# Optimization experiments

Hardware: AMD Instinct MI355X
Metric: run time of the kernel (lower is better)

## Reference

```python
import jax, jax.numpy as jnp
import numpy as np
from jax.scipy.special import logsumexp

EPSILON = 0.01      # Sinkhorn entropic regularization
MAX_ITERATIONS = 50 # Sinkhorn iterations (init kwarg)
NEG_INF = -1e9      # finite stand-in for log(0) to keep grads clean


def setup_inputs() -> dict:
    key = jax.random.key(0)
    k1, k2, k3 = jax.random.split(key, 3)
    B, S, P, D = 8, 2048, 1024, 2
    predictions = jax.random.normal(k1, (B, S, D), dtype=jnp.float32)
    positions = jax.random.normal(k2, (B, P, D), dtype=jnp.float32)
    labels = jax.random.randint(k3, (B, S), 0, P)
    return {"predictions": predictions, "labels": labels, "positions": positions}


def _sinkhorn_loss(predictions, positions, labels):
    B, S, D = predictions.shape
    P = positions.shape[1]
    dt = predictions.dtype

    # target weights = normalized label histogram over the P positions
    w = jnp.zeros((B, P), dt).at[jnp.arange(B)[:, None], labels].add(1.0) / S
    log_a = jnp.full((B, S), -jnp.log(jnp.asarray(S, dt)), dtype=dt)  # uniform source
    log_b = jnp.where(w > 0, jnp.log(jnp.maximum(w, 1e-30)), NEG_INF)

    # squared-Euclidean cost matrix [B, S, P]
    x2 = jnp.sum(predictions * predictions, axis=-1)  # [B,S]
    y2 = jnp.sum(positions * positions, axis=-1)      # [B,P]
    xy = jnp.einsum('bsd,bpd->bsp', predictions, positions)
    C = jnp.maximum(x2[:, :, None] + y2[:, None, :] - 2.0 * xy, 0.0)
    mK = -C / EPSILON  # log-kernel

    def step(carry, _):
        f, g = carry
        f = EPSILON * (log_a - logsumexp(mK + g[:, None, :] / EPSILON, axis=2))
        g = EPSILON * (log_b - logsumexp(mK + f[:, :, None] / EPSILON, axis=1))
        return (f, g), None

    f0 = jnp.zeros((B, S), dt)
    g0 = jnp.zeros((B, P), dt)
    (f, g), _ = jax.lax.scan(step, (f0, g0), None, length=MAX_ITERATIONS)

    # transport plan in log domain; distance = <P, C>
    logT = mK + f[:, :, None] / EPSILON + g[:, None, :] / EPSILON
    dist = jnp.sum(jnp.exp(logT) * C, axis=(1, 2))  # [B]
    return jnp.mean(dist)  # reduction='mean'


def reference(predictions, labels, positions):
    return _sinkhorn_loss(predictions, positions, labels)
```

## Files before the change

### kernel.cpp

```cpp
#include <hip/hip_runtime.h>
#include <math.h>


#define BB 8
#define SS 2048
#define PP 1024
#define NEG_INF -1e9f
#define LOG2S 11.0f
#define ITERS 50
#define K2E 144.269504088896f
#define TWOK 288.539008177792f
#define NBLK 256
#define NTHR 1024

__device__ __forceinline__ float fexp2(float x) {
  return __builtin_amdgcn_exp2f(x);
}
__device__ __forceinline__ float flog2(float x) {
  return __builtin_amdgcn_logf(x);
}

__device__ __forceinline__ float coh_load(const float* p) {
  return __hip_atomic_load((float*)p, __ATOMIC_RELAXED, __HIP_MEMORY_SCOPE_AGENT);
}
__device__ __forceinline__ void coh_store(float* p, float v) {
  __hip_atomic_store(p, v, __ATOMIC_RELAXED, __HIP_MEMORY_SCOPE_AGENT);
}
__device__ __forceinline__ int coh_loadi(const int* p) {
  return __hip_atomic_load((int*)p, __ATOMIC_RELAXED, __HIP_MEMORY_SCOPE_AGENT);
}
__device__ __forceinline__ void coh_storei(int* p, int v) {
  __hip_atomic_store(p, v, __ATOMIC_RELAXED, __HIP_MEMORY_SCOPE_AGENT);
}

__device__ __forceinline__ void batch_barrier(int* slots, int sub, int phase,
                                              int w, int lane) {
  __syncthreads();
  asm volatile("" ::: "memory");
  if (threadIdx.x == 0) coh_storei(&slots[sub], phase);
  if (w == 0) {
    for (;;) {
      int v = (lane < 32) ? coh_loadi(&slots[lane]) : 0x7fffffff;
      if (__all(v >= phase)) break;
      __builtin_amdgcn_s_sleep(1);
    }
  }
  asm volatile("" ::: "memory");
  __syncthreads();
}


__global__ __launch_bounds__(1024) void setup_kernel(
    const int* __restrict__ labels, float* __restrict__ G2,
    float* __restrict__ logb2, int* __restrict__ slots,
    float* __restrict__ out) {
  __shared__ int c[PP];
  int b = blockIdx.x;
  int t = threadIdx.x;
  c[t] = 0;
  __syncthreads();
  atomicAdd(&c[labels[b * SS + t] & (PP - 1)], 1);
  atomicAdd(&c[labels[b * SS + PP + t] & (PP - 1)], 1);
  __syncthreads();
  int cc = c[t];
  logb2[b * PP + t] = (cc > 0) ? (flog2((float)cc) - LOG2S) : NEG_INF;
  G2[b * PP + t] = 0.0f;
  if (t < 32) slots[(b << 5) + t] = 0;
  if (t == 0 && b == 0) out[0] = 0.0f;
}

__global__ __launch_bounds__(1024) void sinkhorn_persist(
    const float* __restrict__ preds, const float* __restrict__ pos,
    const float* __restrict__ logb2, float* __restrict__ F2g,
    float* __restrict__ G2g, int* __restrict__ slots,
    float* __restrict__ out) {
  __shared__ float4 shf[1032];
  __shared__ float4 shg[2064];
  __shared__ float spart;
  const int t = threadIdx.x;
  const int blk = blockIdx.x;
  const int bb = blk >> 5;
  const int sub = blk & 31;
  int* myslots = slots + (bb << 5);
  const float2* pos2 = (const float2*)pos;
  const float2* preds2 = (const float2*)preds;
  float* G2b = G2g + (bb << 10);
  float* F2b = F2g + (bb << 11);

  float yr2, xr2[2];
  {
    float2 y = pos2[(bb << 10) + t];
    yr2 = y.x * y.x + y.y * y.y;
    shf[t + (t >> 7)] = make_float4(y.x, y.y, 0.0f, 0.0f);
  }
#pragma unroll
  for (int k = 0; k < 2; ++k) {
    int e = t + (k << 10);
    float2 x = preds2[(bb << 11) + e];
    xr2[k] = x.x * x.x + x.y * x.y;
    shg[e + (e >> 7)] = make_float4(x.x, x.y, 0.0f, 0.0f);
  }

  const int w = t >> 6, lane = t & 63;
  const int frowb = (blk << 6) + (w << 2);
  float fk0[4], fk1[4], fc0[4];
#pragma unroll
  for (int r = 0; r < 4; ++r) {
    float2 fx = preds2[frowb + r];
    fk0[r] = TWOK * fx.x;
    fk1[r] = TWOK * fx.y;
    fc0[r] = fmaf(K2E, fx.x * fx.x + fx.y * fx.y, -LOG2S);
  }
  const int gcolb = (blk << 5) + (w << 1);
  float gk0[2], gk1[2], gc0[2];
#pragma unroll
  for (int c = 0; c < 2; ++c) {
    float2 gy = pos2[gcolb + c];
    gk0[c] = TWOK * gy.x;
    gk1[c] = TWOK * gy.y;
    gc0[c] = fmaf(K2E, gy.x * gy.x + gy.y * gy.y, logb2[gcolb + c]);
  }

  for (int it = 0; it < ITERS; ++it) {
    shf[t + (t >> 7)].z = fmaf(-K2E, yr2, coh_load(&G2b[t]));
    __syncthreads();
    {
      float m[4], s[4];
#pragma unroll
      for (int r = 0; r < 4; ++r) { m[r] = -3.4e38f; s[r] = 0.0f; }
#pragma unroll
      for (int ch = 0; ch < 2; ++ch) {
        float4 a[8];
#pragma unroll
        for (int i = 0; i < 8; ++i) {
          int e = (((ch << 3) + i) << 6) + lane;
          a[i] = shf[e + (e >> 7)];
        }
#pragma unroll
        for (int r = 0; r < 4; ++r) {
          float u0 = fmaf(fk0[r], a[0].x, fmaf(fk1[r], a[0].y, a[0].z));
          float u1 = fmaf(fk0[r], a[1].x, fmaf(fk1[r], a[1].y, a[1].z));
          float u2 = fmaf(fk0[r], a[2].x, fmaf(fk1[r], a[2].y, a[2].z));
          float u3 = fmaf(fk0[r], a[3].x, fmaf(fk1[r], a[3].y, a[3].z));
          float u4 = fmaf(fk0[r], a[4].x, fmaf(fk1[r], a[4].y, a[4].z));
          float u5 = fmaf(fk0[r], a[5].x, fmaf(fk1[r], a[5].y, a[5].z));
          float u6 = fmaf(fk0[r], a[6].x, fmaf(fk1[r], a[6].y, a[6].z));
          float u7 = fmaf(fk0[r], a[7].x, fmaf(fk1[r], a[7].y, a[7].z));
          float cm = fmaxf(fmaxf(fmaxf(u0, u1), fmaxf(u2, u3)),
                           fmaxf(fmaxf(u4, u5), fmaxf(u6, u7)));
          float mn = fmaxf(m[r], cm);
          float sc = fexp2(m[r] - mn);
          float sum = ((fexp2(u0 - mn) + fexp2(u1 - mn)) +
                       (fexp2(u2 - mn) + fexp2(u3 - mn))) +
                      ((fexp2(u4 - mn) + fexp2(u5 - mn)) +
                       (fexp2(u6 - mn) + fexp2(u7 - mn)));
          s[r] = fmaf(s[r], sc, sum);
          m[r] = mn;
        }
      }
      float fout = 0.0f;
#pragma unroll
      for (int r = 0; r < 4; ++r) {
        float M = m[r];
#pragma unroll
        for (int off = 1; off <= 32; off <<= 1)
          M = fmaxf(M, __shfl_xor(M, off, 64));
        float sr = s[r] * fexp2(m[r] - M);
#pragma unroll
        for (int off = 1; off <= 32; off <<= 1) sr += __shfl_xor(sr, off, 64);
        float v = fc0[r] - M - flog2(sr);
        if (lane == r) fout = v;
      }
      if (lane < 4) coh_store(&F2g[frowb + lane], fout);
    }
    batch_barrier(myslots, sub, 2 * it + 1, w, lane);

#pragma unroll
    for (int k = 0; k < 2; ++k) {
      int e = t + (k << 10);
      shg[e + (e >> 7)].z = fmaf(-K2E, xr2[k], coh_load(&F2b[e]));
    }
    __syncthreads();
    {
      float m[2], s[2];
#pragma unroll
      for (int c = 0; c < 2; ++c) { m[c] = -3.4e38f; s[c] = 0.0f; }
#pragma unroll
      for (int ch = 0; ch < 4; ++ch) {
        float4 a[8];
#pragma unroll
        for (int i = 0; i < 8; ++i) {
          int e = (((ch << 3) + i) << 6) + lane;
          a[i] = shg[e + (e >> 7)];
        }
#pragma unroll
        for (int c = 0; c < 2; ++c) {
          float u0 = fmaf(gk0[c], a[0].x, fmaf(gk1[c], a[0].y, a[0].z));
          float u1 = fmaf(gk0[c], a[1].x, fmaf(gk1[c], a[1].y, a[1].z));
          float u2 = fmaf(gk0[c], a[2].x, fmaf(gk1[c], a[2].y, a[2].z));
          float u3 = fmaf(gk0[c], a[3].x, fmaf(gk1[c], a[3].y, a[3].z));
          float u4 = fmaf(gk0[c], a[4].x, fmaf(gk1[c], a[4].y, a[4].z));
          float u5 = fmaf(gk0[c], a[5].x, fmaf(gk1[c], a[5].y, a[5].z));
          float u6 = fmaf(gk0[c], a[6].x, fmaf(gk1[c], a[6].y, a[6].z));
          float u7 = fmaf(gk0[c], a[7].x, fmaf(gk1[c], a[7].y, a[7].z));
          float cm = fmaxf(fmaxf(fmaxf(u0, u1), fmaxf(u2, u3)),
                           fmaxf(fmaxf(u4, u5), fmaxf(u6, u7)));
          float mn = fmaxf(m[c], cm);
          float sc = fexp2(m[c] - mn);
          float sum = ((fexp2(u0 - mn) + fexp2(u1 - mn)) +
                       (fexp2(u2 - mn) + fexp2(u3 - mn))) +
                      ((fexp2(u4 - mn) + fexp2(u5 - mn)) +
                       (fexp2(u6 - mn) + fexp2(u7 - mn)));
          s[c] = fmaf(s[c], sc, sum);
          m[c] = mn;
        }
      }
      float gout = 0.0f;
#pragma unroll
      for (int c = 0; c < 2; ++c) {
        float M = m[c];
#pragma unroll
        for (int off = 1; off <= 32; off <<= 1)
          M = fmaxf(M, __shfl_xor(M, off, 64));
        float sr = s[c] * fexp2(m[c] - M);
#pragma unroll
        for (int off = 1; off <= 32; off <<= 1) sr += __shfl_xor(sr, off, 64);
        float v = gc0[c] - M - flog2(sr);
        if (lane == c) gout = v;
      }
      if (lane < 2) coh_store(&G2g[gcolb + lane], gout);
    }
    batch_barrier(myslots, sub, 2 * it + 2, w, lane);
  }

  if (t == 0) spart = 0.0f;
  shf[t + (t >> 7)].z = fmaf(-K2E, yr2, coh_load(&G2b[t]));
  __syncthreads();
  float acc = 0.0f;
#pragma unroll
  for (int rr = 0; rr < 4; ++rr) {
    int row = frowb + rr;
    float2 x = preds2[row];
    float x2 = x.x * x.x + x.y * x.y;
    float qx = fmaf(-K2E, x2, coh_load(&F2g[row]));
#pragma unroll
    for (int i = 0; i < 16; ++i) {
      int p = (i << 6) + lane;
      float4 a = shf[p + (p >> 7)];
      float y2 = fmaf(a.x, a.x, a.y * a.y);
      float tt = fmaf(x.y, a.y, x.x * a.x);
      float c = fmaxf(x2 + y2 - 2.0f * tt, 0.0f);
      float v2 = fmaf(TWOK, tt, a.z + qx);
      acc = fmaf(fexp2(v2), c, acc);
    }
  }
#pragma unroll
  for (int off = 32; off; off >>= 1) acc += __shfl_xor(acc, off, 64);
  if (lane == 0) atomicAdd(&spart, acc);
  __syncthreads();
  if (t == 0) atomicAdd(out, spart * (1.0f / (float)BB));
}

extern "C" void kernel_launch(void* const* d_in, const int* in_sizes, int n_in,
                              void* d_out, int out_size, void* d_ws,
                              size_t ws_size, hipStream_t stream) {
  const float* preds = (const float*)d_in[0];
  const int* labels = (const int*)d_in[1];
  const float* pos = (const float*)d_in[2];
  float* out = (float*)d_out;
  char* ws = (char*)d_ws;
  float* G2 = (float*)(ws);
  float* F2 = (float*)(ws + 32768);
  float* logb2 = (float*)(ws + 98304);
  int* slots = (int*)(ws + 131072);

  hipLaunchKernelGGL(setup_kernel, dim3(BB), dim3(1024), 0, stream, labels, G2,
                     logb2, slots, out);
  hipLaunchKernelGGL(sinkhorn_persist, dim3(NBLK), dim3(NTHR), 0, stream,
                     preds, pos, logb2, F2, G2, slots, out);
}
```

Baseline: 611.0 us.

## Double persistent grid to 512 blocks and split row reductions across waves

Raises the persistent Sinkhorn grid from 256 to 512 blocks, so each batch now spans 64 blocks with a 64-slot barrier. Each f-row is now split across two waves and each g-column across four waves, with partial log-sum-exp results merged through a small shared-memory buffer. Per-row and per-column constants are recomputed each iteration to lower register pressure. The goal is more resident waves per CU for better latency hiding. In exchange it adds an extra __syncthreads and merge step per half-iteration, makes the barrier wider, and needs two 1024-thread blocks co-resident per CU, or the spin barrier may deadlock.

```diff
diff --git a/kernel.cpp b/kernel.cpp
--- a/kernel.cpp
+++ b/kernel.cpp
@@ -10,7 +10,7 @@
 #define ITERS 50
 #define K2E 144.269504088896f
 #define TWOK 288.539008177792f
-#define NBLK 256
+#define NBLK 512
 #define NTHR 1024
 
 __device__ __forceinline__ float fexp2(float x) {
@@ -40,7 +40,7 @@
   if (threadIdx.x == 0) coh_storei(&slots[sub], phase);
   if (w == 0) {
     for (;;) {
-      int v = (lane < 32) ? coh_loadi(&slots[lane]) : 0x7fffffff;
+      int v = coh_loadi(&slots[lane]);
       if (__all(v >= phase)) break;
       __builtin_amdgcn_s_sleep(1);
     }
@@ -65,7 +65,7 @@
   int cc = c[t];
   logb2[b * PP + t] = (cc > 0) ? (flog2((float)cc) - LOG2S) : NEG_INF;
   G2[b * PP + t] = 0.0f;
-  if (t < 32) slots[(b << 5) + t] = 0;
+  if (t < 64) slots[(b << 6) + t] = 0;
   if (t == 0 && b == 0) out[0] = 0.0f;
 }
 
@@ -76,12 +76,13 @@
     float* __restrict__ out) {
   __shared__ float4 shf[1032];
   __shared__ float4 shg[2064];
+  __shared__ float2 part[16][4];
   __shared__ float spart;
   const int t = threadIdx.x;
   const int blk = blockIdx.x;
-  const int bb = blk >> 5;
-  const int sub = blk & 31;
-  int* myslots = slots + (bb << 5);
+  const int bb = blk >> 6;
+  const int sub = blk & 63;
+  int* myslots = slots + (bb << 6);
   const float2* pos2 = (const float2*)pos;
   const float2* preds2 = (const float2*)preds;
   float* G2b = G2g + (bb << 10);
@@ -102,38 +103,32 @@
   }
 
   const int w = t >> 6, lane = t & 63;
-  const int frowb = (blk << 6) + (w << 2);
-  float fk0[4], fk1[4], fc0[4];
-#pragma unroll
-  for (int r = 0; r < 4; ++r) {
-    float2 fx = preds2[frowb + r];
-    fk0[r] = TWOK * fx.x;
-    fk1[r] = TWOK * fx.y;
-    fc0[r] = fmaf(K2E, fx.x * fx.x + fx.y * fx.y, -LOG2S);
-  }
-  const int gcolb = (blk << 5) + (w << 1);
-  float gk0[2], gk1[2], gc0[2];
-#pragma unroll
-  for (int c = 0; c < 2; ++c) {
-    float2 gy = pos2[gcolb + c];
-    gk0[c] = TWOK * gy.x;
-    gk1[c] = TWOK * gy.y;
-    gc0[c] = fmaf(K2E, gy.x * gy.x + gy.y * gy.y, logb2[gcolb + c]);
-  }
+  const int rg = w >> 1, th = w & 1;
+  const int frowb = (bb << 11) + (sub << 5) + (rg << 2);
+  const int cg = w >> 2, tq = w & 3;
+  const int gcolb = (bb << 10) + (sub << 4) + (cg << 2);
 
   for (int it = 0; it < ITERS; ++it) {
     shf[t + (t >> 7)].z = fmaf(-K2E, yr2, coh_load(&G2b[t]));
     __syncthreads();
     {
+      float fk0[4], fk1[4], fc0[4];
+#pragma unroll
+      for (int r = 0; r < 4; ++r) {
+        float2 fx = preds2[frowb + r];
+        fk0[r] = TWOK * fx.x;
+        fk1[r] = TWOK * fx.y;
+        fc0[r] = fmaf(K2E, fx.x * fx.x + fx.y * fx.y, -LOG2S);
+      }
       float m[4], s[4];
 #pragma unroll
       for (int r = 0; r < 4; ++r) { m[r] = -3.4e38f; s[r] = 0.0f; }
 #pragma unroll
       for (int ch = 0; ch < 2; ++ch) {
-        float4 a[8];
-#pragma unroll
-        for (int i = 0; i < 8; ++i) {
-          int e = (((ch << 3) + i) << 6) + lane;
+        float4 a[4];
+#pragma unroll
+        for (int i = 0; i < 4; ++i) {
+          int e = (th << 9) + (((ch << 2) + i) << 6) + lane;
           a[i] = shf[e + (e >> 7)];
         }
 #pragma unroll
@@ -142,23 +137,16 @@
           float u1 = fmaf(fk0[r], a[1].x, fmaf(fk1[r], a[1].y, a[1].z));
           float u2 = fmaf(fk0[r], a[2].x, fmaf(fk1[r], a[2].y, a[2].z));
           float u3 = fmaf(fk0[r], a[3].x, fmaf(fk1[r], a[3].y, a[3].z));
-          float u4 = fmaf(fk0[r], a[4].x, fmaf(fk1[r], a[4].y, a[4].z));
-          float u5 = fmaf(fk0[r], a[5].x, fmaf(fk1[r], a[5].y, a[5].z));
-          float u6 = fmaf(fk0[r], a[6].x, fmaf(fk1[r], a[6].y, a[6].z));
-          float u7 = fmaf(fk0[r], a[7].x, fmaf(fk1[r], a[7].y, a[7].z));
-          float cm = fmaxf(fmaxf(fmaxf(u0, u1), fmaxf(u2, u3)),
-                           fmaxf(fmaxf(u4, u5), fmaxf(u6, u7)));
+          float cm = fmaxf(fmaxf(u0, u1), fmaxf(u2, u3));
           float mn = fmaxf(m[r], cm);
           float sc = fexp2(m[r] - mn);
-          float sum = ((fexp2(u0 - mn) + fexp2(u1 - mn)) +
-                       (fexp2(u2 - mn) + fexp2(u3 - mn))) +
-                      ((fexp2(u4 - mn) + fexp2(u5 - mn)) +
-                       (fexp2(u6 - mn) + fexp2(u7 - mn)));
+          float sum = (fexp2(u0 - mn) + fexp2(u1 - mn)) +
+                      (fexp2(u2 - mn) + fexp2(u3 - mn));
           s[r] = fmaf(s[r], sc, sum);
           m[r] = mn;
         }
       }
-      float fout = 0.0f;
+      float2 myp = make_float2(0.0f, 0.0f);
 #pragma unroll
       for (int r = 0; r < 4; ++r) {
         float M = m[r];
@@ -168,10 +156,17 @@
         float sr = s[r] * fexp2(m[r] - M);
 #pragma unroll
         for (int off = 1; off <= 32; off <<= 1) sr += __shfl_xor(sr, off, 64);
-        float v = fc0[r] - M - flog2(sr);
-        if (lane == r) fout = v;
-      }
-      if (lane < 4) coh_store(&F2g[frowb + lane], fout);
+        if (lane == r) myp = make_float2(M - fc0[r], sr);
+      }
+      if (lane < 4) part[w][lane] = myp;
+    }
+    __syncthreads();
+    if (th == 0 && lane < 4) {
+      float2 p0 = part[w][lane];
+      float2 p1 = part[w + 1][lane];
+      float M = fmaxf(p0.x, p1.x);
+      float S = p0.y * fexp2(p0.x - M) + p1.y * fexp2(p1.x - M);
+      coh_store(&F2g[frowb + lane], -M - flog2(S));
     }
     batch_barrier(myslots, sub, 2 * it + 1, w, lane);
 
@@ -182,42 +177,43 @@
     }
     __syncthreads();
     {
-      float m[2], s[2];
-#pragma unroll
-      for (int c = 0; c < 2; ++c) { m[c] = -3.4e38f; s[c] = 0.0f; }
-#pragma unroll
-      for (int ch = 0; ch < 4; ++ch) {
-        float4 a[8];
-#pragma unroll
-        for (int i = 0; i < 8; ++i) {
-          int e = (((ch << 3) + i) << 6) + lane;
+      float gk0[4], gk1[4], gc0[4];
+#pragma unroll
+      for (int c = 0; c < 4; ++c) {
+        float2 gy = pos2[gcolb + c];
+        gk0[c] = TWOK * gy.x;
+        gk1[c] = TWOK * gy.y;
+        gc0[c] = fmaf(K2E, gy.x * gy.x + gy.y * gy.y, logb2[gcolb + c]);
+      }
+      float m[4], s[4];
+#pragma unroll
+      for (int c = 0; c < 4; ++c) { m[c] = -3.4e38f; s[c] = 0.0f; }
+#pragma unroll
+      for (int ch = 0; ch < 2; ++ch) {
+        float4 a[4];
+#pragma unroll
+        for (int i = 0; i < 4; ++i) {
+          int e = (tq << 9) + (((ch << 2) + i) << 6) + lane;
           a[i] = shg[e + (e >> 7)];
         }
 #pragma unroll
-        for (int c = 0; c < 2; ++c) {
+        for (int c = 0; c < 4; ++c) {
           float u0 = fmaf(gk0[c], a[0].x, fmaf(gk1[c], a[0].y, a[0].z));
           float u1 = fmaf(gk0[c], a[1].x, fmaf(gk1[c], a[1].y, a[1].z));
           float u2 = fmaf(gk0[c], a[2].x, fmaf(gk1[c], a[2].y, a[2].z));
           float u3 = fmaf(gk0[c], a[3].x, fmaf(gk1[c], a[3].y, a[3].z));
-          float u4 = fmaf(gk0[c], a[4].x, fmaf(gk1[c], a[4].y, a[4].z));
-          float u5 = fmaf(gk0[c], a[5].x, fmaf(gk1[c], a[5].y, a[5].z));
-          float u6 = fmaf(gk0[c], a[6].x, fmaf(gk1[c], a[6].y, a[6].z));
-          float u7 = fmaf(gk0[c], a[7].x, fmaf(gk1[c], a[7].y, a[7].z));
-          float cm = fmaxf(fmaxf(fmaxf(u0, u1), fmaxf(u2, u3)),
-                           fmaxf(fmaxf(u4, u5), fmaxf(u6, u7)));
+          float cm = fmaxf(fmaxf(u0, u1), fmaxf(u2, u3));
           float mn = fmaxf(m[c], cm);
           float sc = fexp2(m[c] - mn);
-          float sum = ((fexp2(u0 - mn) + fexp2(u1 - mn)) +
-                       (fexp2(u2 - mn) + fexp2(u3 - mn))) +
-                      ((fexp2(u4 - mn) + fexp2(u5 - mn)) +
-                       (fexp2(u6 - mn) + fexp2(u7 - mn)));
+          float sum = (fexp2(u0 - mn) + fexp2(u1 - mn)) +
+                      (fexp2(u2 - mn) + fexp2(u3 - mn));
           s[c] = fmaf(s[c], sc, sum);
           m[c] = mn;
         }
       }
-      float gout = 0.0f;
-#pragma unroll
-      for (int c = 0; c < 2; ++c) {
+      float2 myp = make_float2(0.0f, 0.0f);
+#pragma unroll
+      for (int c = 0; c < 4; ++c) {
         float M = m[c];
 #pragma unroll
         for (int off = 1; off <= 32; off <<= 1)
@@ -225,10 +221,20 @@
         float sr = s[c] * fexp2(m[c] - M);
 #pragma unroll
         for (int off = 1; off <= 32; off <<= 1) sr += __shfl_xor(sr, off, 64);
-        float v = gc0[c] - M - flog2(sr);
-        if (lane == c) gout = v;
-      }
-      if (lane < 2) coh_store(&G2g[gcolb + lane], gout);
+        if (lane == c) myp = make_float2(M - gc0[c], sr);
+      }
+      if (lane < 4) part[w][lane] = myp;
+    }
+    __syncthreads();
+    if (tq == 0 && lane < 4) {
+      float2 p0 = part[w][lane];
+      float2 p1 = part[w + 1][lane];
+      float2 p2 = part[w + 2][lane];
+      float2 p3 = part[w + 3][lane];
+      float M = fmaxf(fmaxf(p0.x, p1.x), fmaxf(p2.x, p3.x));
+      float S = p0.y * fexp2(p0.x - M) + p1.y * fexp2(p1.x - M) +
+                p2.y * fexp2(p2.x - M) + p3.y * fexp2(p3.x - M);
+      coh_store(&G2g[gcolb + lane], -M - flog2(S));
     }
     batch_barrier(myslots, sub, 2 * it + 2, w, lane);
   }
@@ -238,8 +244,8 @@
   __syncthreads();
   float acc = 0.0f;
 #pragma unroll
-  for (int rr = 0; rr < 4; ++rr) {
-    int row = frowb + rr;
+  for (int rr = 0; rr < 2; ++rr) {
+    int row = (bb << 11) + (sub << 5) + (w << 1) + rr;
     float2 x = preds2[row];
     float x2 = x.x * x.x + x.y * x.y;
     float qx = fmaf(-K2E, x2, coh_load(&F2g[row]));
```

Result: slower. 1.316 ms (+115.4%).
